# Performance work log

Measured on AMD Instinct MI355X. Metric: run time of the kernel, lower is better.

Reference implementation:

```python
import jax, jax.numpy as jnp
import numpy as np
from jax import lax

DN = ('NHWC', 'HWIO', 'NHWC')
OUTPUT_STRIDE = 2
PEAK_THRESHOLD = 0.2


def setup_inputs() -> dict:
    key = jax.random.key(0)
    k1, k2, k3 = jax.random.split(key, 3)
    crops = jax.random.normal(k1, (128, 192, 192, 1), dtype=jnp.float32)
    # simple confmap backbone: stride-2 conv -> relu -> 3x3 conv to 17 nodes
    W1 = jax.random.normal(k2, (3, 3, 1, 32), dtype=jnp.float32) * 0.1
    b1 = jnp.zeros((32,), dtype=jnp.float32)
    W2 = jax.random.normal(k3, (3, 3, 32, 17), dtype=jnp.float32) * 0.1
    b2 = jnp.zeros((17,), dtype=jnp.float32)
    return {"crops": crops, "W1": W1, "b1": b1, "W2": W2, "b2": b2}


def _confmaps(crops, W1, b1, W2, b2):
    # keras_model forward: (B, 192, 192, 1) -> (B, 96, 96, 17), output_stride = 2
    h = lax.conv_general_dilated(crops, W1, (2, 2), 'SAME', dimension_numbers=DN) + b1
    h = jax.nn.relu(h)
    cms = lax.conv_general_dilated(h, W2, (1, 1), 'SAME', dimension_numbers=DN) + b2
    return cms


def _find_global_peaks_local(cms, threshold):
    # cms: (B, H, W, N) -> peaks (B, N, 2) in (x, y), vals (B, N)
    B, H, W, N = cms.shape
    cm = jnp.transpose(cms, (0, 3, 1, 2)).reshape(B, N, H * W)  # (B, N, HW)
    flat_idx = jnp.argmax(cm, axis=-1)                           # (B, N)
    vals = jnp.take_along_axis(cm, flat_idx[..., None], axis=-1)[..., 0]
    yi = flat_idx // W
    xi = flat_idx % W

    def gather(yy, xx):
        yy = jnp.clip(yy, 0, H - 1)
        xx = jnp.clip(xx, 0, W - 1)
        return jnp.take_along_axis(cm, (yy * W + xx)[..., None], axis=-1)[..., 0]

    # quarter-pixel local gradient offset (refinement='local')
    dx = 0.25 * jnp.sign(gather(yi, xi + 1) - gather(yi, xi - 1))
    dy = 0.25 * jnp.sign(gather(yi + 1, xi) - gather(yi - 1, xi))

    pts = jnp.stack([xi.astype(cm.dtype) + dx, yi.astype(cm.dtype) + dy], axis=-1)
    pts = jnp.where(vals[..., None] >= threshold, pts, jnp.nan)
    return pts, vals


def reference(crops, W1, b1, W2, b2):
    # preprocess: inputs already float grayscale, input_scale=1.0 -> identity
    cms = _confmaps(crops, W1, b1, W2, b2)
    peak_points, peak_vals = _find_global_peaks_local(cms, PEAK_THRESHOLD)
    peak_points = peak_points * OUTPUT_STRIDE  # adjust to input image grid
    # pack (x, y, val) into one array: (B, nodes, 3)
    return jnp.concatenate([peak_points, peak_vals[..., None]], axis=-1)
```

## Files before the change

kernel.cpp:

```cpp
#include <hip/hip_runtime.h>


#define NCH 17
#define C1 32
#define TW 24
#define TH 32
#define HT_W 26
#define HT_H 34
#define HSTR 28
#define IN_W 53
#define IN_H 69
#define CG 4
#define NG 8

typedef float v2f __attribute__((ext_vector_type(2)));

__device__ __forceinline__ unsigned long long pack_key(float v, unsigned flat) {
    unsigned ub = __float_as_uint(v);
    ub = (ub & 0x80000000u) ? ~ub : (ub | 0x80000000u);
    return ((unsigned long long)ub << 32) | (unsigned)(~flat);
}

__global__ __launch_bounds__(256, 4) void conv_peaks_kernel(
    const float* __restrict__ crops, const float* __restrict__ W1g,
    const float* __restrict__ b1g, const float* __restrict__ W2g,
    const float* __restrict__ b2g, unsigned long long* __restrict__ peaks) {
    __shared__ float s_in[IN_H * IN_W];
    __shared__ __align__(16) float s_h[CG * HT_H * HSTR];

    const int t = threadIdx.x;
    const int b = blockIdx.y;
    const int ty0 = (blockIdx.x >> 2) * TH;
    const int tx0 = (blockIdx.x & 3) * TW;
    const int iy0 = 2 * ty0 - 2;
    const int ix0 = 2 * tx0 - 2;
    const float* cb = crops + b * 192 * 192;

    for (int p = t; p < IN_H * IN_W; p += 256) {
        int r = p / IN_W, cc = p - r * IN_W;
        int iy = iy0 + r, ix = ix0 + cc;
        float v = 0.f;
        if (iy >= 0 && ix >= 0 && iy < 192 && ix < 192) v = cb[iy * 192 + ix];
        s_in[p] = v;
    }

    const int ly = t >> 3;
    const int lx0 = (t & 7) * 3;
    v2f acc2[8][3];
    float acc1[3];
#pragma unroll
    for (int m = 0; m < 8; ++m)
#pragma unroll
        for (int p = 0; p < 3; ++p) acc2[m][p] = (v2f)(0.f);
#pragma unroll
    for (int p = 0; p < 3; ++p) acc1[p] = 0.f;

#pragma unroll 1
    for (int g = 0; g < NG; ++g) {
        __syncthreads();

        for (int p = t; p < HT_H * HT_W; p += 256) {
            int r = p / HT_W, cc = p - r * HT_W;
            int hy = ty0 - 1 + r, hx = tx0 - 1 + cc;
            bool valid = (hy >= 0) && (hy < 96) && (hx >= 0) && (hx < 96);
            float in9[9];
#pragma unroll
            for (int q = 0; q < 9; ++q)
                in9[q] = s_in[(2 * r + q / 3) * IN_W + (2 * cc + q % 3)];
#pragma unroll
            for (int cl = 0; cl < CG; ++cl) {
                int c = g * CG + cl;
                float a = b1g[c];
#pragma unroll
                for (int q = 0; q < 9; ++q) a = fmaf(in9[q], W1g[q * C1 + c], a);
                a = valid ? fmaxf(a, 0.f) : 0.f;
                s_h[cl * (HT_H * HSTR) + r * HSTR + cc] = a;
            }
        }
        __syncthreads();

#pragma unroll 1
        for (int cl = 0; cl < CG; ++cl) {
            float hrow[3][5];
            const float* hp = s_h + cl * (HT_H * HSTR) + ly * HSTR + lx0;
#pragma unroll
            for (int r = 0; r < 3; ++r)
#pragma unroll
                for (int j = 0; j < 5; ++j) hrow[r][j] = hp[r * HSTR + j];
            const int c = g * CG + cl;
#pragma unroll
            for (int k = 0; k < 9; ++k) {
                const int ky = k / 3, kx = k - ky * 3;
                const float* wb = W2g + (k * C1 + c) * NCH;
                float w[NCH];
#pragma unroll
                for (int n = 0; n < NCH; ++n) w[n] = wb[n];
                v2f wp[8];
#pragma unroll
                for (int m = 0; m < 8; ++m) wp[m] = (v2f){w[2 * m], w[2 * m + 1]};
#pragma unroll
                for (int p = 0; p < 3; ++p) {
                    const float h = hrow[ky][kx + p];
                    const v2f hh = {h, h};
#pragma unroll
                    for (int m = 0; m < 8; ++m)
                        acc2[m][p] = __builtin_elementwise_fma(hh, wp[m], acc2[m][p]);
                    acc1[p] = fmaf(h, w[16], acc1[p]);
                }
            }
        }
    }

    const int yg = ty0 + ly, xg = tx0 + lx0;
    const int lane = t & 63;
#pragma unroll
    for (int n = 0; n < NCH; ++n) {
        const float bb = b2g[n];
        float v_[3];
#pragma unroll
        for (int p = 0; p < 3; ++p)
            v_[p] = ((n < 16) ? acc2[n >> 1][p][n & 1] : acc1[p]) + bb;
        unsigned long long pk = pack_key(v_[0], (unsigned)(yg * 96 + xg));
#pragma unroll
        for (int p = 1; p < 3; ++p) {
            unsigned long long o = pack_key(v_[p], (unsigned)(yg * 96 + xg + p));
            if (o > pk) pk = o;
        }
#pragma unroll
        for (int off = 32; off; off >>= 1) {
            unsigned long long o = __shfl_down(pk, off, 64);
            if (o > pk) pk = o;
        }
        if (lane == 0) atomicMax(&peaks[b * NCH + n], pk);
    }
}

__global__ __launch_bounds__(64) void refine_kernel(
    const float* __restrict__ crops, const float* __restrict__ W1g,
    const float* __restrict__ b1g, const float* __restrict__ W2g,
    const unsigned long long* __restrict__ peaks, float* __restrict__ out) {
    const int bn = blockIdx.x;
    const int b = bn / NCH, n = bn % NCH;
    const int lane = threadIdx.x;

    unsigned long long pk = peaks[bn];
    unsigned key = (unsigned)(pk >> 32);
    unsigned fbits = (key & 0x80000000u) ? (key ^ 0x80000000u) : ~key;
    float val = __uint_as_float(fbits);
    int flat = (int)(~(unsigned)(pk & 0xffffffffu));
    int yi = flat / 96, xi = flat - yi * 96;

    const int j = lane >> 4;
    int yy = yi + ((j == 2) ? 1 : 0) - ((j == 3) ? 1 : 0);
    int xx = xi + ((j == 0) ? 1 : 0) - ((j == 1) ? 1 : 0);
    yy = min(max(yy, 0), 95);
    xx = min(max(xx, 0), 95);

    const float* cb = crops + b * 192 * 192;
    float pat[7][7];
#pragma unroll
    for (int r = 0; r < 7; ++r) {
        int iy = 2 * yy - 2 + r;
#pragma unroll
        for (int s = 0; s < 7; ++s) {
            int ix = 2 * xx - 2 + s;
            pat[r][s] = (iy >= 0 && iy < 192 && ix >= 0 && ix < 192)
                            ? cb[iy * 192 + ix] : 0.f;
        }
    }

    float part = 0.f;
#pragma unroll
    for (int ci = 0; ci < 2; ++ci) {
        const int c = (lane & 15) + ci * 16;
        const float bias = b1g[c];
        float w1[9];
#pragma unroll
        for (int q = 0; q < 9; ++q) w1[q] = W1g[q * C1 + c];
#pragma unroll
        for (int dy = 0; dy < 3; ++dy) {
#pragma unroll
            for (int dx = 0; dx < 3; ++dx) {
                int hy = yy - 1 + dy, hx = xx - 1 + dx;
                if (hy >= 0 && hy < 96 && hx >= 0 && hx < 96) {
                    float a = bias;
#pragma unroll
                    for (int qy = 0; qy < 3; ++qy)
#pragma unroll
                        for (int qx = 0; qx < 3; ++qx)
                            a = fmaf(pat[2 * dy + qy][2 * dx + qx],
                                     w1[qy * 3 + qx], a);
                    float hval = fmaxf(a, 0.f);
                    part = fmaf(hval, W2g[((dy * 3 + dx) * C1 + c) * NCH + n], part);
                }
            }
        }
    }
    for (int off = 8; off; off >>= 1) part += __shfl_down(part, off, 16);
    float g0 = __shfl(part, 0, 64);
    float g1 = __shfl(part, 16, 64);
    float g2 = __shfl(part, 32, 64);
    float g3 = __shfl(part, 48, 64);

    if (lane == 0) {
        float d0 = g0 - g1, d1 = g2 - g3;
        float sx = (d0 > 0.f) ? 1.f : ((d0 < 0.f) ? -1.f : 0.f);
        float sy = (d1 > 0.f) ? 1.f : ((d1 < 0.f) ? -1.f : 0.f);
        float px = ((float)xi + 0.25f * sx) * 2.f;
        float py = ((float)yi + 0.25f * sy) * 2.f;
        if (!(val >= 0.2f)) {
            px = __int_as_float(0x7fc00000);
            py = __int_as_float(0x7fc00000);
        }
        out[bn * 3 + 0] = px;
        out[bn * 3 + 1] = py;
        out[bn * 3 + 2] = val;
    }
}

extern "C" void kernel_launch(void* const* d_in, const int* in_sizes, int n_in,
                              void* d_out, int out_size, void* d_ws, size_t ws_size,
                              hipStream_t stream) {
    const float* crops = (const float*)d_in[0];
    const float* W1 = (const float*)d_in[1];
    const float* b1 = (const float*)d_in[2];
    const float* W2 = (const float*)d_in[3];
    const float* b2 = (const float*)d_in[4];
    float* out = (float*)d_out;
    unsigned long long* peaks = (unsigned long long*)d_ws;

    hipMemsetAsync(d_ws, 0, 128 * NCH * sizeof(unsigned long long), stream);

    dim3 gridB(12, 128);
    conv_peaks_kernel<<<gridB, 256, 0, stream>>>(crops, W1, b1, W2, b2, peaks);
    refine_kernel<<<128 * NCH, 64, 0, stream>>>(crops, W1, b1, W2, peaks, out);
}
```

Before: 207.7 us.

## Halve channel group, precompute conv1 offsets, use inline packed FMA with scalar weights

Splits layer-1 channels into groups of two instead of four, shrinking shared memory for the hidden tile and raising the launch-bounds occupancy target to six blocks per SM. Pixel offsets and validity masks for the conv1 stage are computed once outside the channel loop, and conv1 weights are loaded once per group. Conv2 inner loop is restructured to load hidden rows per ky and issue v_pk_fma_f32 via inline asm with weights in SGPRs to avoid VGPR broadcasting. This doubles the number of barriers and group iterations, and the higher occupancy target may force register spills.

```diff
diff --git a/kernel.cpp b/kernel.cpp
--- a/kernel.cpp
+++ b/kernel.cpp
@@ -10,8 +10,9 @@
 #define HSTR 28
 #define IN_W 53
 #define IN_H 69
-#define CG 4
-#define NG 8
+#define CG 2
+#define NG 16
+#define NHPX (HT_H * HT_W)
 
 typedef float v2f __attribute__((ext_vector_type(2)));
 
@@ -21,7 +22,7 @@
     return ((unsigned long long)ub << 32) | (unsigned)(~flat);
 }
 
-__global__ __launch_bounds__(256, 4) void conv_peaks_kernel(
+__global__ __launch_bounds__(256, 6) void conv_peaks_kernel(
     const float* __restrict__ crops, const float* __restrict__ W1g,
     const float* __restrict__ b1g, const float* __restrict__ W2g,
     const float* __restrict__ b2g, unsigned long long* __restrict__ peaks) {
@@ -44,6 +45,19 @@
         s_in[p] = v;
     }
 
+    int in_off[4], out_off[4];
+    float vf[4];
+#pragma unroll
+    for (int i = 0; i < 4; ++i) {
+        int p = t + i * 256;
+        int r = p / HT_W, cc = p - r * HT_W;
+        int hy = ty0 - 1 + r, hx = tx0 - 1 + cc;
+        bool valid = (hy >= 0) && (hy < 96) && (hx >= 0) && (hx < 96);
+        vf[i] = valid ? 1.f : 0.f;
+        in_off[i] = 2 * r * IN_W + 2 * cc;
+        out_off[i] = r * HSTR + cc;
+    }
+
     const int ly = t >> 3;
     const int lx0 = (t & 7) * 3;
     v2f acc2[8][3];
@@ -59,53 +73,69 @@
     for (int g = 0; g < NG; ++g) {
         __syncthreads();
 
-        for (int p = t; p < HT_H * HT_W; p += 256) {
-            int r = p / HT_W, cc = p - r * HT_W;
-            int hy = ty0 - 1 + r, hx = tx0 - 1 + cc;
-            bool valid = (hy >= 0) && (hy < 96) && (hx >= 0) && (hx < 96);
-            float in9[9];
-#pragma unroll
-            for (int q = 0; q < 9; ++q)
-                in9[q] = s_in[(2 * r + q / 3) * IN_W + (2 * cc + q % 3)];
-#pragma unroll
-            for (int cl = 0; cl < CG; ++cl) {
-                int c = g * CG + cl;
-                float a = b1g[c];
-#pragma unroll
-                for (int q = 0; q < 9; ++q) a = fmaf(in9[q], W1g[q * C1 + c], a);
-                a = valid ? fmaxf(a, 0.f) : 0.f;
-                s_h[cl * (HT_H * HSTR) + r * HSTR + cc] = a;
+        {
+            const float b10 = b1g[2 * g], b11 = b1g[2 * g + 1];
+            float w10[9], w11[9];
+#pragma unroll
+            for (int q = 0; q < 9; ++q) {
+                w10[q] = W1g[q * C1 + 2 * g];
+                w11[q] = W1g[q * C1 + 2 * g + 1];
+            }
+#pragma unroll
+            for (int i = 0; i < 4; ++i) {
+                if (i < 3 || t < NHPX - 768) {
+                    const float* ip = s_in + in_off[i];
+                    float in9[9];
+#pragma unroll
+                    for (int qy = 0; qy < 3; ++qy)
+#pragma unroll
+                        for (int qx = 0; qx < 3; ++qx)
+                            in9[qy * 3 + qx] = ip[qy * IN_W + qx];
+                    float a0 = b10, a1 = b11;
+#pragma unroll
+                    for (int q = 0; q < 9; ++q) {
+                        a0 = fmaf(in9[q], w10[q], a0);
+                        a1 = fmaf(in9[q], w11[q], a1);
+                    }
+                    a0 = fmaxf(a0, 0.f) * vf[i];
+                    a1 = fmaxf(a1, 0.f) * vf[i];
+                    s_h[out_off[i]] = a0;
+                    s_h[HT_H * HSTR + out_off[i]] = a1;
+                }
             }
         }
         __syncthreads();
 
-#pragma unroll 1
+#pragma unroll
         for (int cl = 0; cl < CG; ++cl) {
-            float hrow[3][5];
+            const int c = g * CG + cl;
             const float* hp = s_h + cl * (HT_H * HSTR) + ly * HSTR + lx0;
 #pragma unroll
-            for (int r = 0; r < 3; ++r)
-#pragma unroll
-                for (int j = 0; j < 5; ++j) hrow[r][j] = hp[r * HSTR + j];
-            const int c = g * CG + cl;
-#pragma unroll
-            for (int k = 0; k < 9; ++k) {
-                const int ky = k / 3, kx = k - ky * 3;
-                const float* wb = W2g + (k * C1 + c) * NCH;
-                float w[NCH];
-#pragma unroll
-                for (int n = 0; n < NCH; ++n) w[n] = wb[n];
-                v2f wp[8];
-#pragma unroll
-                for (int m = 0; m < 8; ++m) wp[m] = (v2f){w[2 * m], w[2 * m + 1]};
-#pragma unroll
-                for (int p = 0; p < 3; ++p) {
-                    const float h = hrow[ky][kx + p];
-                    const v2f hh = {h, h};
-#pragma unroll
-                    for (int m = 0; m < 8; ++m)
-                        acc2[m][p] = __builtin_elementwise_fma(hh, wp[m], acc2[m][p]);
-                    acc1[p] = fmaf(h, w[16], acc1[p]);
+            for (int ky = 0; ky < 3; ++ky) {
+                float hr[5];
+#pragma unroll
+                for (int j = 0; j < 5; ++j) hr[j] = hp[ky * HSTR + j];
+                v2f hb[5];
+#pragma unroll
+                for (int j = 0; j < 5; ++j) hb[j] = (v2f){hr[j], hr[j]};
+#pragma unroll
+                for (int kx = 0; kx < 3; ++kx) {
+                    const int k = ky * 3 + kx;
+                    const float* wb = W2g + (k * C1 + c) * NCH;
+                    float w[NCH];
+#pragma unroll
+                    for (int n = 0; n < NCH; ++n) w[n] = wb[n];
+#pragma unroll
+                    for (int p = 0; p < 3; ++p) {
+#pragma unroll
+                        for (int m = 0; m < 8; ++m) {
+                            v2f wp = (v2f){w[2 * m], w[2 * m + 1]};
+                            asm("v_pk_fma_f32 %0, %1, %2, %0"
+                                : "+v"(acc2[m][p])
+                                : "v"(hb[kx + p]), "s"(wp));
+                        }
+                        acc1[p] = fmaf(hr[kx + p], w[16], acc1[p]);
+                    }
                 }
             }
         }
```

New measurement: 218.8 us. +5.4%, slower.
